# Kernel tuning notes

Hardware: AMD Instinct MI355X
Metric: run time of the kernel (lower is better)

The kernel has to match this reference:

```python
import jax, jax.numpy as jnp
import numpy as np

IMG_H = 800
IMG_W = 800
LEVEL_HW = [(200, 200), (100, 100), (50, 50), (25, 25), (13, 13)]
SIZES = [32.0, 64.0, 128.0, 256.0, 512.0]
RATIOS = np.array([0.5, 1.0, 2.0])
PRE_NMS = 1000     # rpn_pre_nms_top_n_test
POST_NMS = 1000    # rpn_post_nms_top_n_test
NMS_THRESH = 0.7
MIN_SIZE = 1e-3
BBOX_CLAMP = float(np.log(1000.0 / 16.0))  # torchvision BoxCoder clamp


def _make_anchors():
    """torchvision AnchorGenerator: 3 anchors/location, (h,w,a)-major order."""
    per_level = []
    for (H, W), size in zip(LEVEL_HW, SIZES):
        h_r = np.sqrt(RATIOS)
        w_r = 1.0 / h_r
        ws = w_r * size
        hs = h_r * size
        base = np.round(np.stack([-ws, -hs, ws, hs], axis=1) / 2.0)  # [3,4]
        stride_y = IMG_H // H
        stride_x = IMG_W // W
        shift_x = np.arange(W) * stride_x
        shift_y = np.arange(H) * stride_y
        yy, xx = np.meshgrid(shift_y, shift_x, indexing='ij')
        shifts = np.stack([xx.ravel(), yy.ravel(), xx.ravel(), yy.ravel()], axis=1)
        a = (shifts[:, None, :] + base[None, :, :]).reshape(-1, 4)  # [H*W*3,4]
        per_level.append(jnp.asarray(a, jnp.float32))
    return per_level


def _conv(x, w, b, pad):
    y = jax.lax.conv_general_dilated(
        x, w, window_strides=(1, 1), padding=[(pad, pad), (pad, pad)],
        dimension_numbers=('NCHW', 'OIHW', 'NCHW'))
    return y + b[None, :, None, None]


def _rpn_forward(feats, conv_w, conv_b, cls_w, cls_b, bbox_w, bbox_b):
    anchors_l = _make_anchors()
    boxes_list, scores_list, lvls_list = [], [], []
    for lvl, f in enumerate(feats):
        t = jax.nn.relu(_conv(f, conv_w, conv_b, 1))
        logits = _conv(t, cls_w, cls_b, 0)     # [1,3,H,W]
        deltas = _conv(t, bbox_w, bbox_b, 0)   # [1,12,H,W]
        H, W = f.shape[2], f.shape[3]
        s = logits[0].transpose(1, 2, 0).reshape(-1)                       # (h,w,a)
        d = deltas[0].reshape(3, 4, H, W).transpose(2, 3, 0, 1).reshape(-1, 4)
        k = min(PRE_NMS, s.shape[0])
        topv, topi = jax.lax.top_k(s, k)
        a = anchors_l[lvl][topi]
        dd = d[topi]
        # BoxCoder.decode, weights=(1,1,1,1)
        w_ = a[:, 2] - a[:, 0]
        h_ = a[:, 3] - a[:, 1]
        cx = a[:, 0] + 0.5 * w_
        cy = a[:, 1] + 0.5 * h_
        dx, dy = dd[:, 0], dd[:, 1]
        dw = jnp.minimum(dd[:, 2], BBOX_CLAMP)
        dh = jnp.minimum(dd[:, 3], BBOX_CLAMP)
        pcx = dx * w_ + cx
        pcy = dy * h_ + cy
        pw = jnp.exp(dw) * w_
        ph = jnp.exp(dh) * h_
        bx = jnp.stack([pcx - 0.5 * pw, pcy - 0.5 * ph,
                        pcx + 0.5 * pw, pcy + 0.5 * ph], axis=1)
        boxes_list.append(bx)
        scores_list.append(topv)
        lvls_list.append(jnp.full((k,), float(lvl), jnp.float32))
    boxes = jnp.concatenate(boxes_list)    # [N,4], N=4507
    scores = jnp.concatenate(scores_list)
    lvls = jnp.concatenate(lvls_list)
    # clip to image
    boxes = jnp.stack([boxes[:, 0].clip(0.0, IMG_W), boxes[:, 1].clip(0.0, IMG_H),
                       boxes[:, 2].clip(0.0, IMG_W), boxes[:, 3].clip(0.0, IMG_H)], axis=1)
    valid = ((boxes[:, 2] - boxes[:, 0]) >= MIN_SIZE) & ((boxes[:, 3] - boxes[:, 1]) >= MIN_SIZE)
    # batched NMS: offset boxes per level so cross-level IoU is zero
    off = lvls * (IMG_W + 1.0)
    ob = boxes + off[:, None]
    N = boxes.shape[0]
    order = jnp.argsort(-scores)
    b = ob[order]
    rb = boxes[order]
    s = scores[order]
    v = valid[order]
    area = (b[:, 2] - b[:, 0]) * (b[:, 3] - b[:, 1])
    lt = jnp.maximum(b[:, None, :2], b[None, :, :2])
    rbr = jnp.minimum(b[:, None, 2:], b[None, :, 2:])
    wh = jnp.clip(rbr - lt, 0.0)
    inter = wh[..., 0] * wh[..., 1]
    iou = inter / (area[:, None] + area[None, :] - inter)  # [N,N]
    idxs = jnp.arange(N)
    def body(i, keep):
        sup = keep[i] & (iou[i] > NMS_THRESH) & (idxs > i)
        return keep & ~sup
    keep = jax.lax.fori_loop(0, N, body, v)
    final_scores = jnp.where(keep, s, -jnp.inf)
    _, ki = jax.lax.top_k(final_scores, POST_NMS)
    return rb[ki]  # [POST_NMS, 4] proposals (padded to fixed size)


def setup_inputs() -> dict:
    key = jax.random.key(0)
    ks = jax.random.split(key, 12)
    inp = {}
    for i, (name, (H, W)) in enumerate(zip(['feat0', 'feat1', 'feat2', 'feat3', 'feat4'], LEVEL_HW)):
        inp[name] = jax.random.normal(ks[i], (1, 256, H, W), jnp.float32)
    inp['conv_w'] = jax.random.normal(ks[5], (256, 256, 3, 3), jnp.float32) * 0.02
    inp['conv_b'] = jnp.zeros((256,), jnp.float32)
    inp['cls_w'] = jax.random.normal(ks[6], (3, 256, 1, 1), jnp.float32) * 0.02
    inp['cls_b'] = jnp.zeros((3,), jnp.float32)
    inp['bbox_w'] = jax.random.normal(ks[7], (12, 256, 1, 1), jnp.float32) * 0.02
    inp['bbox_b'] = jnp.zeros((12,), jnp.float32)
    return inp


def reference(feat0, feat1, feat2, feat3, feat4, conv_w, conv_b, cls_w, cls_b, bbox_w, bbox_b):
    feats = [feat0, feat1, feat2, feat3, feat4]
    return _rpn_forward(feats, conv_w, conv_b, cls_w, cls_b, bbox_w, bbox_b)
```

## Files before the change

kernel.cpp:

```cpp
#include <hip/hip_runtime.h>
#include <cmath>

typedef unsigned int u32;
typedef unsigned long long u64;
typedef _Float16 f16;
typedef _Float16 f16x8 __attribute__((ext_vector_type(8)));
typedef float f32x4 __attribute__((ext_vector_type(4)));

typedef __attribute__((address_space(1))) const unsigned int gu32;
typedef __attribute__((address_space(3))) unsigned int lu32;

#define NCAND 4507
#define WORDS 71
#define ROWS_AL (WORDS * 64)
#define TOTS 159882

__constant__ int c_W[5]      = {200, 100, 50, 25, 13};
__constant__ int c_stride[5] = {4, 8, 16, 32, 61};
__constant__ int c_Nl[5]     = {120000, 30000, 7500, 1875, 507};
__constant__ int c_soff[5]   = {0, 120000, 150000, 157500, 159375};
__constant__ int c_k[5]      = {1000, 1000, 1000, 1000, 507};

__constant__ int cv_boff[6]  = {0, 625, 794, 843, 859, 863};

struct DecParams { float b[5][3][4]; };
struct FeatPtrs { const float* p[5]; };

__device__ __forceinline__ u32 flipf(float f) {
    u32 u = __float_as_uint(f);
    return (u & 0x80000000u) ? ~u : (u | 0x80000000u);
}

constexpr size_t AL(size_t x) { return (x + 255) & ~(size_t)255; }
constexpr size_t OFF_WHI    = 0;
constexpr size_t OFF_WLO    = AL(OFF_WHI + 1179648);
constexpr size_t OFF_HEADW  = AL(OFF_WLO + 1179648);
constexpr size_t OFF_HEADB  = AL(OFF_HEADW + 3840 * 4);
constexpr size_t OFF_SCORES = AL(OFF_HEADB + 64);
constexpr size_t OFF_DELTAS = AL(OFF_SCORES + (size_t)TOTS * 4);
constexpr size_t OFF_KEY    = AL(OFF_DELTAS + (size_t)TOTS * 16);
constexpr size_t OFF_SBOX   = AL(OFF_KEY + (size_t)NCAND * 8);
constexpr size_t OFF_SOB    = AL(OFF_SBOX + (size_t)NCAND * 16);
constexpr size_t OFF_SVAL   = AL(OFF_SOB + (size_t)NCAND * 16);
constexpr size_t OFF_MASK   = AL(OFF_SVAL + (size_t)NCAND * 4);
constexpr size_t OFF_KEEP   = AL(OFF_MASK + (size_t)ROWS_AL * WORDS * 8);
constexpr size_t OFF_GHIST  = AL(OFF_KEEP + WORDS * 8);

__global__ __launch_bounds__(256) void k_prep(
    const float* __restrict__ cw, const float* __restrict__ clsw,
    const float* __restrict__ clsb, const float* __restrict__ bw,
    const float* __restrict__ bb, f16* __restrict__ whi, f16* __restrict__ wlo,
    float* __restrict__ headw, float* __restrict__ headb, u32* __restrict__ ghist) {
    int i = blockIdx.x * 256 + threadIdx.x;
    if (i < 589824) {
        int blk = i >> 13;
        int within = i & 8191;
        int co = within >> 5;
        int rem = within & 31;
        int slot = rem >> 3, j = rem & 7;
        int chunk = blk / 9, kk = blk - chunk * 9;
        int ky = kk / 3, kx = kk - ky * 3;
        int g = slot ^ ((co >> 1) & 3);
        int ci = (chunk << 5) | (g << 3) | j;
        float w = cw[(((co << 8) + ci) * 3 + ky) * 3 + kx];
        f16 hi = (f16)w;
        whi[i] = hi;
        wlo[i] = (f16)((w - (float)hi) * 2048.0f);
    }
    if (i < 3840) {
        int h = i >> 8, ci = i & 255;
        headw[i] = (h < 3) ? clsw[h * 256 + ci] : bw[(h - 3) * 256 + ci];
    }
    if (i < 15) headb[i] = (i < 3) ? clsb[i] : bb[i - 3];
    if (i < 1280) ghist[i] = 0;
}

__global__ __launch_bounds__(512) void k_conv(
    FeatPtrs fp, const f16* __restrict__ whi, const f16* __restrict__ wlo,
    const float* __restrict__ convb, const float* __restrict__ headw,
    const float* __restrict__ headb, float* __restrict__ scores,
    float* __restrict__ deltas) {
    __shared__ float4 smq[4896];
    char* smb = (char*)smq;
    const int tid = threadIdx.x;
    const int lane = tid & 63, wv = tid >> 6;
    const int l15 = lane & 15, l4 = lane >> 4;

    const int bid = blockIdx.x;
    int l = 0;
#pragma unroll
    for (int q = 1; q < 5; q++) if (bid >= cv_boff[q]) l = q;
    const int H = c_W[l], W = H;
    const int soff = c_soff[l];
    const float* __restrict__ in = fp.p[l];
    const int t = bid - cv_boff[l];
    const int tilesx = (W + 7) >> 3;
    const int tx = t % tilesx, ty = t / tilesx;
    const int x0 = tx * 8, y0 = ty * 8;
    const int HW = H * W;

    int rbase0, rbase1, rbase2, rbase3;
    {
        int rr = l15 >> 3;
        rbase0 = (0 + rr) * 640; rbase1 = (2 + rr) * 640;
        rbase2 = (4 + rr) * 640; rbase3 = (6 + rr) * 640;
    }
    int colx0, colx1, colx2;
    {
        int c = lane & 7;
        int p0 = c, p1 = c + 1, p2 = c + 2;
        colx0 = p0 * 64 + ((l4 ^ ((p0 >> 1) & 3)) << 4);
        colx1 = p1 * 64 + ((l4 ^ ((p1 >> 1) & 3)) << 4);
        colx2 = p2 * 64 + ((l4 ^ ((p2 >> 1) & 3)) << 4);
    }
    int bco0 = wv * 32 + l15, bco1 = wv * 32 + 16 + l15;
    const int boff0 = bco0 * 64 + ((l4 ^ ((bco0 >> 1) & 3)) << 4);
    const int boff1 = bco1 * 64 + ((l4 ^ ((bco1 >> 1) & 3)) << 4);

    f32x4 acc1[4][2], acc2[4][2];
#pragma unroll
    for (int mt = 0; mt < 4; mt++)
#pragma unroll
        for (int nt = 0; nt < 2; nt++) {
            acc1[mt][nt] = (f32x4)0.0f;
            acc2[mt][nt] = (f32x4)0.0f;
        }

    auto stagePatch = [&](int chunk) {
        const int c0 = chunk << 5;
        f16* ph = (f16*)smb;
        f16* pl = (f16*)(smb + 6400);
        for (int e = tid; e < 3200; e += 512) {
            int py = e / 320, rem = e - py * 320;
            int px = rem >> 5, ci = rem & 31;
            int gy = y0 - 1 + py, gx = x0 - 1 + px;
            float v = 0.f;
            if (gy >= 0 && gy < H && gx >= 0 && gx < W)
                v = in[(c0 + ci) * HW + gy * W + gx];
            f16 hi = (f16)v;
            int widx = py * 320 + px * 32 + (((ci >> 3) ^ ((px >> 1) & 3)) << 3) + (ci & 7);
            ph[widx] = hi;
            pl[widx] = (f16)((v - (float)hi) * 2048.0f);
        }
    };
    auto issueB = [&](int sidx, int buf) {
        const char* gh = (const char*)whi + (size_t)sidx * 16384;
        const char* gl = (const char*)wlo + (size_t)sidx * 16384;
        char* dh = smb + 12800 + buf * 32768;
        char* dl = dh + 16384;
#pragma unroll
        for (int q = 0; q < 2; q++) {
            int i1 = (wv * 2 + q) * 1024;
            __builtin_amdgcn_global_load_lds((gu32*)(gh + i1 + lane * 16), (lu32*)(dh + i1), 16, 0, 0);
            __builtin_amdgcn_global_load_lds((gu32*)(gl + i1 + lane * 16), (lu32*)(dl + i1), 16, 0, 0);
        }
    };

// ... 34 lines not shown
                    acc2[1][nt] = __builtin_amdgcn_mfma_f32_16x16x32_f16(ah1, vbl, acc2[1][nt], 0, 0, 0);
                    acc2[1][nt] = __builtin_amdgcn_mfma_f32_16x16x32_f16(al1, vbh, acc2[1][nt], 0, 0, 0);
                    acc1[2][nt] = __builtin_amdgcn_mfma_f32_16x16x32_f16(ah2, vbh, acc1[2][nt], 0, 0, 0);
                    acc2[2][nt] = __builtin_amdgcn_mfma_f32_16x16x32_f16(ah2, vbl, acc2[2][nt], 0, 0, 0);
                    acc2[2][nt] = __builtin_amdgcn_mfma_f32_16x16x32_f16(al2, vbh, acc2[2][nt], 0, 0, 0);
                    acc1[3][nt] = __builtin_amdgcn_mfma_f32_16x16x32_f16(ah3, vbh, acc1[3][nt], 0, 0, 0);
                    acc2[3][nt] = __builtin_amdgcn_mfma_f32_16x16x32_f16(ah3, vbl, acc2[3][nt], 0, 0, 0);
                    acc2[3][nt] = __builtin_amdgcn_mfma_f32_16x16x32_f16(al3, vbh, acc2[3][nt], 0, 0, 0);
                }
            }
            __syncthreads();
        }
    }

    const float INV2048 = 4.8828125e-4f;
    {
        float cb0 = convb[bco0], cb1 = convb[bco1];
#pragma unroll
        for (int mt = 0; mt < 4; mt++)
#pragma unroll
            for (int nt = 0; nt < 2; nt++) {
                float cb = nt ? cb1 : cb0;
#pragma unroll
                for (int r = 0; r < 4; r++) {
                    float tv = acc1[mt][nt][r] + acc2[mt][nt][r] * INV2048 + cb;
                    acc1[mt][nt][r] = tv > 0.f ? tv : 0.f;
                }
            }
    }

    float* part = (float*)smb;
    for (int hc = 0; hc < 15; hc += 3) {
        float hw3[3][2];
#pragma unroll
        for (int h3 = 0; h3 < 3; h3++) {
            hw3[h3][0] = headw[(hc + h3) * 256 + bco0];
            hw3[h3][1] = headw[(hc + h3) * 256 + bco1];
        }
#pragma unroll
        for (int mt = 0; mt < 4; mt++)
#pragma unroll
            for (int r = 0; r < 4; r++) {
                float p0 = 0.f, p1 = 0.f, p2 = 0.f;
#pragma unroll
                for (int nt = 0; nt < 2; nt++) {
                    float tv = acc1[mt][nt][r];
                    p0 = fmaf(hw3[0][nt], tv, p0);
                    p1 = fmaf(hw3[1][nt], tv, p1);
                    p2 = fmaf(hw3[2][nt], tv, p2);
                }
                p0 += __shfl_xor(p0, 1); p0 += __shfl_xor(p0, 2); p0 += __shfl_xor(p0, 4); p0 += __shfl_xor(p0, 8);
                p1 += __shfl_xor(p1, 1); p1 += __shfl_xor(p1, 2); p1 += __shfl_xor(p1, 4); p1 += __shfl_xor(p1, 8);
                p2 += __shfl_xor(p2, 1); p2 += __shfl_xor(p2, 2); p2 += __shfl_xor(p2, 4); p2 += __shfl_xor(p2, 8);
                if (l15 == 0) {
                    int px = mt * 16 + l4 * 4 + r;
                    part[(wv * 64 + px) * 3 + 0] = p0;
                    part[(wv * 64 + px) * 3 + 1] = p1;
                    part[(wv * 64 + px) * 3 + 2] = p2;
                }
            }
        __syncthreads();
        if (tid < 192) {
            int px = tid / 3, h3 = tid % 3;
            int h = hc + h3;
            float sum = 0.f;
#pragma unroll
            for (int g = 0; g < 8; g++) sum += part[(g * 64 + px) * 3 + h3];
            sum += headb[h];
            int gy = y0 + (px >> 3), gx = x0 + (px & 7);
            if (gy < H && gx < W) {
                int pix = gy * W + gx;
                if (h < 3) {
                    scores[soff + pix * 3 + h] = sum;
                } else {
                    int ch2 = h - 3;
                    deltas[((size_t)(soff + pix * 3 + (ch2 >> 2))) * 4 + (ch2 & 3)] = sum;
                }
            }
        }
        __syncthreads();
    }
}

__global__ __launch_bounds__(256) void k_hist(
    const float* __restrict__ scores, u32* __restrict__ ghist) {
    __shared__ u32 lh[1280];
    for (int i = threadIdx.x; i < 1280; i += 256) lh[i] = 0;
    __syncthreads();
    const int gsz = gridDim.x * 256;
    for (int i = blockIdx.x * 256 + threadIdx.x; i < TOTS; i += gsz) {
        int l = (i >= 120000) + (i >= 150000) + (i >= 157500) + (i >= 159375);
        u32 b = flipf(scores[i]) >> 24;
        atomicAdd(&lh[l * 256 + b], 1u);
    }
    __syncthreads();
    for (int i = threadIdx.x; i < 1280; i += 256) {
        u32 v = lh[i];
        if (v) atomicAdd(&ghist[i], v);
    }
}

__global__ __launch_bounds__(1024) void k_topk2(
    const float* __restrict__ scores, const u32* __restrict__ ghist,
    u64* __restrict__ key, u64* __restrict__ scr1, u64* __restrict__ scr2) {
    const int l = blockIdx.x;
    const int Nl = c_Nl[l], off = c_soff[l], k = c_k[l];
    const int base = l * 1000;
    const int tid = threadIdx.x;
    const int lane = tid & 63;
    const u32 lshift = (u32)l << 24;
    __shared__ u32 hist[256];
    __shared__ u32 sh_sel, sh_cn, sh_b, sh_m;
    __shared__ u32 tiebuf[2048];

    if (k == Nl) {
        for (int i = tid; i < Nl; i += 1024) {
            u32 k32 = flipf(scores[off + i]);
            key[base + i] = ((u64)(~k32) << 32) | (u64)(lshift | (u32)i);
        }
        return;
    }
    if (tid == 0) {
        sh_sel = 0; sh_cn = 0;
        u32 cum = 0, m0 = (u32)k;
        for (int b = 255; b >= 0; --b) {
            u32 c = ghist[l * 256 + b];
            if (cum + c >= m0) { sh_b = (u32)b; sh_m = m0 - cum; break; }
            cum += c;
        }
    }
    __syncthreads();
    u32 b0 = sh_b, m = sh_m;

    u64* C = scr1 + off;
    for (int i = tid; i < Nl; i += 1024) {
        u32 k32 = flipf(scores[off + i]);
        u32 b = k32 >> 24;
        bool sel = b > b0, tie = (b == b0);
        u64 msk = __ballot(sel);
        if (msk) {
            int ldr = __builtin_ctzll(msk);
            u32 bs = 0;
            if (lane == ldr) bs = atomicAdd(&sh_sel, (u32)__popcll(msk));
            bs = __shfl(bs, ldr);
            if (sel) {
                u32 slot = bs + (u32)__popcll(msk & ((1ull << lane) - 1ull));
                key[base + slot] = ((u64)(~k32) << 32) | (u64)(lshift | (u32)i);
            }
        }
        msk = __ballot(tie);
        if (msk) {
            int ldr = __builtin_ctzll(msk);
            u32 bs = 0;
            if (lane == ldr) bs = atomicAdd(&sh_cn, (u32)__popcll(msk));
            bs = __shfl(bs, ldr);
            if (tie) {
                u32 slot = bs + (u32)__popcll(msk & ((1ull << lane) - 1ull));
                C[slot] = ((u64)k32 << 32) | (u64)(u32)i;
            }
        }
    }
    __syncthreads();
    u32 n = sh_cn;
    __syncthreads();

    u64* curb = C;
    u64* nxtb = scr2 + off;
    for (int p = 1; p <= 3; ++p) {
        const int shift = 56 - 8 * p;
        for (int b = tid; b < 256; b += 1024) hist[b] = 0;
        if (tid == 0) sh_cn = 0;
        __syncthreads();
        for (u32 j = tid; j < n; j += 1024)
            atomicAdd(&hist[(u32)(curb[j] >> shift) & 255u], 1u);
        __syncthreads();
        if (tid == 0) {
            u32 cum = 0;
            for (int b = 255; b >= 0; --b) {
                u32 c = hist[b];
                if (cum + c >= m) { sh_b = (u32)b; sh_m = m - cum; break; }
                cum += c;
            }
        }
        __syncthreads();
        u32 bp = sh_b; m = sh_m;
        for (u32 j = tid; j < n; j += 1024) {
            u64 e = curb[j];
            u32 b = (u32)(e >> shift) & 255u;
            bool sel = b > bp, tie = (b == bp);
            u64 msk = __ballot(sel);
            if (msk) {
                int ldr = __builtin_ctzll(msk);
                u32 bs = 0;
                if (lane == ldr) bs = atomicAdd(&sh_sel, (u32)__popcll(msk));
                bs = __shfl(bs, ldr);
                if (sel) {
                    u32 slot = bs + (u32)__popcll(msk & ((1ull << lane) - 1ull));
                    u32 k32 = (u32)(e >> 32);
                    key[base + slot] = ((u64)(~k32) << 32) | (u64)(lshift | (u32)(e & 0xFFFFFFu));
                }
            }
            msk = __ballot(tie);
            if (msk) {
                int ldr = __builtin_ctzll(msk);
                u32 bs = 0;
                if (lane == ldr) bs = atomicAdd(&sh_cn, (u32)__popcll(msk));
                bs = __shfl(bs, ldr);
                if (tie) {
                    u32 slot = bs + (u32)__popcll(msk & ((1ull << lane) - 1ull));
                    nxtb[slot] = e;
                }
            }
        }
        __syncthreads();
        n = sh_cn;
        __syncthreads();
        u64* tmp = curb; curb = nxtb; nxtb = tmp;
    }

    u32 nsel = sh_sel;
    u32 kt = (u32)(curb[0] >> 32);
    if (n == m) {
        for (u32 j = tid; j < n; j += 1024) {
            u64 e = curb[j];
            key[base + nsel + j] = ((u64)(~kt) << 32) | (u64)(lshift | (u32)(e & 0xFFFFFFu));
        }
    } else {
        for (u32 j = tid; j < 2048; j += 1024) tiebuf[j] = 0xFFFFFFFFu;
        __syncthreads();
        for (u32 j = tid; j < n && j < 2048; j += 1024) tiebuf[j] = (u32)(curb[j] & 0xFFFFFFu);
        __syncthreads();
        for (u32 ksz = 2; ksz <= 2048; ksz <<= 1) {
            for (u32 jj = ksz >> 1; jj > 0; jj >>= 1) {
                for (u32 i2 = tid; i2 < 2048; i2 += 1024) {
                    u32 ixj = i2 ^ jj;
                    if (ixj > i2) {
                        u32 a = tiebuf[i2], b = tiebuf[ixj];
                        bool up = ((i2 & ksz) == 0);
                        if ((a > b) == up) { tiebuf[i2] = b; tiebuf[ixj] = a; }
                    }
                }
                __syncthreads();
            }
        }
        for (u32 j = tid; j < m; j += 1024)
            key[base + nsel + j] = ((u64)(~kt) << 32) | (u64)(lshift | tiebuf[j]);
    }
}

__global__ __launch_bounds__(1024) void k_sort(
    const u64* __restrict__ key, const float* __restrict__ deltas, DecParams P,
    float* __restrict__ sboxes, float* __restrict__ sob, u32* __restrict__ svalid) {
    __shared__ u64 sk[8192];
    const int tid = threadIdx.x;
    for (int i = tid; i < 8192; i += 1024) sk[i] = (i < NCAND) ? key[i] : ~0ull;
    __syncthreads();
    for (u32 ksz = 2; ksz <= 8192; ksz <<= 1) {
        for (u32 j = ksz >> 1; j > 0; j >>= 1) {
            for (u32 i = tid; i < 8192; i += 1024) {
                u32 ixj = i ^ j;
                if (ixj > i) {
                    u64 a = sk[i], b = sk[ixj];
                    bool up = ((i & ksz) == 0);
                    if ((a > b) == up) { sk[i] = b; sk[ixj] = a; }
                }
            }
            __syncthreads();
        }
    }
    const float CLAMP = 4.135166556742356f;
    for (int s = tid; s < NCAND; s += 1024) {
        u32 info = (u32)sk[s];
        int l = info >> 24, idx = info & 0xFFFFFF;
        int W = c_W[l], st = c_stride[l];
        int a = idx % 3, pix = idx / 3;
        int x = pix % W, y = pix / W;
        float ax1 = x * st + P.b[l][a][0];
        float ay1 = y * st + P.b[l][a][1];
        float ax2 = x * st + P.b[l][a][2];
        float ay2 = y * st + P.b[l][a][3];
        float w_ = ax2 - ax1, h_ = ay2 - ay1;
        float cx = ax1 + 0.5f * w_, cy = ay1 + 0.5f * h_;
        const float* d = deltas + ((size_t)(c_soff[l] + idx)) * 4;
        float dx = d[0], dy = d[1];
        float dw = fminf(d[2], CLAMP), dh = fminf(d[3], CLAMP);
        float pcx = dx * w_ + cx, pcy = dy * h_ + cy;
        float pw = expf(dw) * w_, ph = expf(dh) * h_;
        float x1 = pcx - 0.5f * pw, y1 = pcy - 0.5f * ph;
        float x2 = pcx + 0.5f * pw, y2 = pcy + 0.5f * ph;
        x1 = fminf(fmaxf(x1, 0.f), 800.f); y1 = fminf(fmaxf(y1, 0.f), 800.f);
        x2 = fminf(fmaxf(x2, 0.f), 800.f); y2 = fminf(fmaxf(y2, 0.f), 800.f);
        u32 vv = (x2 - x1 >= 0.001f && y2 - y1 >= 0.001f) ? 1u : 0u;
        float offv = (float)l * 801.0f;
        sboxes[s * 4 + 0] = x1; sboxes[s * 4 + 1] = y1;
        sboxes[s * 4 + 2] = x2; sboxes[s * 4 + 3] = y2;
        sob[s * 4 + 0] = x1 + offv; sob[s * 4 + 1] = y1 + offv;
        sob[s * 4 + 2] = x2 + offv; sob[s * 4 + 3] = y2 + offv;
        svalid[s] = vv;
    }
}

__global__ __launch_bounds__(256) void k_mask(
    const float* __restrict__ sob, u64* __restrict__ mask) {
    int gid = blockIdx.x * 256 + threadIdx.x;
    const int total = NCAND * WORDS;
    if (gid >= total) return;
    int i = gid / WORDS, w = gid - i * WORDS;
    float bx1 = sob[i * 4], by1 = sob[i * 4 + 1], bx2 = sob[i * 4 + 2], by2 = sob[i * 4 + 3];
    float ai = (bx2 - bx1) * (by2 - by1);
    u64 bits = 0;
    int j0 = w * 64;
    for (int b = 0; b < 64; b++) {
        int j = j0 + b;
        if (j < NCAND && j > i) {
            float cx1 = sob[j * 4], cy1 = sob[j * 4 + 1], cx2 = sob[j * 4 + 2], cy2 = sob[j * 4 + 3];
            float lt0 = fmaxf(bx1, cx1), lt1 = fmaxf(by1, cy1);
            float rb0 = fminf(bx2, cx2), rb1 = fminf(by2, cy2);
            float ww = fmaxf(rb0 - lt0, 0.f), hh = fmaxf(rb1 - lt1, 0.f);
            float inter = ww * hh;
            float aj = (cx2 - cx1) * (cy2 - cy1);
            float u = ai + aj - inter;
            float iou = inter / u;
            if (iou > 0.7f) bits |= (1ull << b);
        }
    }
    mask[(size_t)i * WORDS + w] = bits;
}

__global__ __launch_bounds__(1024) void k_scan(
    const u64* __restrict__ mask, const u32* __restrict__ svalid,
    const float* __restrict__ sboxes, float* __restrict__ out) {
    __shared__ u64 keep[WORDS];
    __shared__ u32 ormL[WORDS], ormH[WORDS];
    __shared__ u32 sc[1024];
    const int tid = threadIdx.x;
    if (tid < WORDS) {
        u64 w0 = 0;
        for (int b = 0; b < 64; b++) {
// ... 21 lines not shown
        }
        __syncthreads();
        u64 kw = keep[t];
        int nW = WORDS - 1 - t;
        for (int task = tid; task < 64 * nW; task += 1024) {
            int r = task / nW, w = t + 1 + (task - r * nW);
            if ((kw >> r) & 1ull) {
                u64 mrow = mask[(size_t)(t * 64 + r) * WORDS + w];
                if (mrow) {
                    atomicOr(&ormL[w], (u32)mrow);
                    atomicOr(&ormH[w], (u32)(mrow >> 32));
                }
            }
        }
        __syncthreads();
        if (tid > t && tid < WORDS) {
            keep[tid] &= ~(((u64)ormH[tid] << 32) | (u64)ormL[tid]);
            ormL[tid] = 0; ormH[tid] = 0;
        }
        __syncthreads();
    }
    const int i0 = tid * 5;
    u32 cnt = 0;
    for (int e = 0; e < 5; e++) {
        int i = i0 + e;
        if (i < NCAND) cnt += (u32)((keep[i >> 6] >> (i & 63)) & 1ull);
    }
    sc[tid] = cnt;
    __syncthreads();
    for (int off = 1; off < 1024; off <<= 1) {
        u32 v = (tid >= off) ? sc[tid - off] : 0;
        __syncthreads();
        sc[tid] += v;
        __syncthreads();
    }
    u32 incl = sc[tid];
    u32 total = sc[1023];
    u32 kr = incl - cnt;
    for (int e = 0; e < 5; e++) {
        int i = i0 + e;
        if (i < NCAND) {
            bool kp = (keep[i >> 6] >> (i & 63)) & 1ull;
            if (kp) {
                if (kr < 1000u) {
                    out[kr * 4 + 0] = sboxes[i * 4 + 0];
                    out[kr * 4 + 1] = sboxes[i * 4 + 1];
                    out[kr * 4 + 2] = sboxes[i * 4 + 2];
                    out[kr * 4 + 3] = sboxes[i * 4 + 3];
                }
                kr++;
            } else {
                u32 slot = total + (u32)i - kr;
                if (slot < 1000u) {
                    out[slot * 4 + 0] = sboxes[i * 4 + 0];
                    out[slot * 4 + 1] = sboxes[i * 4 + 1];
                    out[slot * 4 + 2] = sboxes[i * 4 + 2];
                    out[slot * 4 + 3] = sboxes[i * 4 + 3];
                }
            }
        }
    }
}

extern "C" void kernel_launch(void* const* d_in, const int* in_sizes, int n_in,
                              void* d_out, int out_size, void* d_ws, size_t ws_size,
                              hipStream_t stream) {
    (void)in_sizes; (void)n_in; (void)out_size; (void)ws_size;
    FeatPtrs fp;
    for (int i = 0; i < 5; i++) fp.p[i] = (const float*)d_in[i];
    const float* conv_w = (const float*)d_in[5];
    const float* conv_b = (const float*)d_in[6];
    const float* cls_w  = (const float*)d_in[7];
    const float* cls_b  = (const float*)d_in[8];
    const float* bbox_w = (const float*)d_in[9];
    const float* bbox_b = (const float*)d_in[10];

    char* ws = (char*)d_ws;
    f16*   whi    = (f16*)(ws + OFF_WHI);
    f16*   wlo    = (f16*)(ws + OFF_WLO);
    float* headw  = (float*)(ws + OFF_HEADW);
    float* headb  = (float*)(ws + OFF_HEADB);
    float* scores = (float*)(ws + OFF_SCORES);
    float* deltas = (float*)(ws + OFF_DELTAS);
    u64*   key    = (u64*)(ws + OFF_KEY);
    float* sboxes = (float*)(ws + OFF_SBOX);
    float* sob    = (float*)(ws + OFF_SOB);
    u32*   svalid = (u32*)(ws + OFF_SVAL);
    u64*   maskp  = (u64*)(ws + OFF_MASK);
    u32*   ghist  = (u32*)(ws + OFF_GHIST);
    u64*   scr1   = maskp;
    u64*   scr2   = maskp + TOTS;

    k_prep<<<2304, 256, 0, stream>>>(conv_w, cls_w, cls_b, bbox_w, bbox_b,
                                     whi, wlo, headw, headb, ghist);

    k_conv<<<863, 512, 0, stream>>>(fp, whi, wlo, conv_b, headw, headb, scores, deltas);

    k_hist<<<256, 256, 0, stream>>>(scores, ghist);
    k_topk2<<<5, 1024, 0, stream>>>(scores, ghist, key, scr1, scr2);

    DecParams dp;
    {
        const double sz[5] = {32.0, 64.0, 128.0, 256.0, 512.0};
        const double rt[3] = {0.5, 1.0, 2.0};
        for (int l = 0; l < 5; l++)
            for (int a = 0; a < 3; a++) {
                double hr = sqrt(rt[a]);
                double wr = 1.0 / hr;
                double w = wr * sz[l], h = hr * sz[l];
                dp.b[l][a][0] = (float)nearbyint(-w / 2.0);
                dp.b[l][a][1] = (float)nearbyint(-h / 2.0);
                dp.b[l][a][2] = (float)nearbyint(w / 2.0);
                dp.b[l][a][3] = (float)nearbyint(h / 2.0);
            }
    }
    k_sort<<<1, 1024, 0, stream>>>(key, deltas, dp, sboxes, sob, svalid);
    k_mask<<<(NCAND * WORDS + 255) / 256, 256, 0, stream>>>(sob, maskp);
    k_scan<<<1, 1024, 0, stream>>>(maskp, svalid, sboxes, (float*)d_out);
}
```

Baseline: 980.9 us.

## Fuse histogram, per-level top-k selection and global sort into one kernel

Merges the histogram kernel, the 5-block radix top-k kernel and the single-block bitonic sort into one single-block kernel. Selected keys are written straight into shared memory instead of going through a global key buffer. Launch overhead and the global round trip are removed, and the per-level tie passes exit early when the ties are already resolved. The cost is that the 160K-element histogram and the candidate selection for all levels now run serially on one workgroup rather than across 256 plus 5 blocks.

```diff
diff --git a/kernel.cpp b/kernel.cpp
--- a/kernel.cpp
+++ b/kernel.cpp
@@ -38,19 +38,17 @@
 constexpr size_t OFF_HEADB  = AL(OFF_HEADW + 3840 * 4);
 constexpr size_t OFF_SCORES = AL(OFF_HEADB + 64);
 constexpr size_t OFF_DELTAS = AL(OFF_SCORES + (size_t)TOTS * 4);
-constexpr size_t OFF_KEY    = AL(OFF_DELTAS + (size_t)TOTS * 16);
-constexpr size_t OFF_SBOX   = AL(OFF_KEY + (size_t)NCAND * 8);
+constexpr size_t OFF_SBOX   = AL(OFF_DELTAS + (size_t)TOTS * 16);
 constexpr size_t OFF_SOB    = AL(OFF_SBOX + (size_t)NCAND * 16);
 constexpr size_t OFF_SVAL   = AL(OFF_SOB + (size_t)NCAND * 16);
 constexpr size_t OFF_MASK   = AL(OFF_SVAL + (size_t)NCAND * 4);
 constexpr size_t OFF_KEEP   = AL(OFF_MASK + (size_t)ROWS_AL * WORDS * 8);
-constexpr size_t OFF_GHIST  = AL(OFF_KEEP + WORDS * 8);
 
 __global__ __launch_bounds__(256) void k_prep(
     const float* __restrict__ cw, const float* __restrict__ clsw,
     const float* __restrict__ clsb, const float* __restrict__ bw,
     const float* __restrict__ bb, f16* __restrict__ whi, f16* __restrict__ wlo,
-    float* __restrict__ headw, float* __restrict__ headb, u32* __restrict__ ghist) {
+    float* __restrict__ headw, float* __restrict__ headb) {
     int i = blockIdx.x * 256 + threadIdx.x;
     if (i < 589824) {
         int blk = i >> 13;
@@ -72,7 +70,6 @@
         headw[i] = (h < 3) ? clsw[h * 256 + ci] : bw[(h - 3) * 256 + ci];
     }
     if (i < 15) headb[i] = (i < 3) ? clsb[i] : bb[i - 3];
-    if (i < 1280) ghist[i] = 0;
 }
 
 __global__ __launch_bounds__(512) void k_conv(
@@ -273,178 +270,184 @@
     }
 }
 
-__global__ __launch_bounds__(256) void k_hist(
-    const float* __restrict__ scores, u32* __restrict__ ghist) {
-    __shared__ u32 lh[1280];
-    for (int i = threadIdx.x; i < 1280; i += 256) lh[i] = 0;
-    __syncthreads();
-    const int gsz = gridDim.x * 256;
-    for (int i = blockIdx.x * 256 + threadIdx.x; i < TOTS; i += gsz) {
-        int l = (i >= 120000) + (i >= 150000) + (i >= 157500) + (i >= 159375);
-        u32 b = flipf(scores[i]) >> 24;
-        atomicAdd(&lh[l * 256 + b], 1u);
-    }
-    __syncthreads();
-    for (int i = threadIdx.x; i < 1280; i += 256) {
-        u32 v = lh[i];
-        if (v) atomicAdd(&ghist[i], v);
-    }
-}
-
-__global__ __launch_bounds__(1024) void k_topk2(
-    const float* __restrict__ scores, const u32* __restrict__ ghist,
-    u64* __restrict__ key, u64* __restrict__ scr1, u64* __restrict__ scr2) {
-    const int l = blockIdx.x;
-    const int Nl = c_Nl[l], off = c_soff[l], k = c_k[l];
-    const int base = l * 1000;
+__global__ __launch_bounds__(1024) void k_select(
+    const float* __restrict__ scores, const float* __restrict__ deltas, DecParams P,
+    float* __restrict__ sboxes, float* __restrict__ sob, u32* __restrict__ svalid,
+    u64* __restrict__ scr1, u64* __restrict__ scr2) {
+    __shared__ u64 sk[8192];
+    __shared__ u32 hist[1280];
+    __shared__ u32 tiebuf[2048];
+    __shared__ u32 sh_b0[5], sh_m[5], sh_sel[5], sh_cnt[5], sh_t1, sh_t2;
     const int tid = threadIdx.x;
     const int lane = tid & 63;
-    const u32 lshift = (u32)l << 24;
-    __shared__ u32 hist[256];
-    __shared__ u32 sh_sel, sh_cn, sh_b, sh_m;
-    __shared__ u32 tiebuf[2048];
-
-    if (k == Nl) {
+
+    for (int i = tid; i < 1280; i += 1024) hist[i] = 0;
+    __syncthreads();
+    for (int bi = 0; bi < TOTS; bi += 1024) {
+        int i = bi + tid;
+        bool valid = i < TOTS;
+        u32 bin = 0;
+        if (valid) {
+            int l = (i >= 120000) + (i >= 150000) + (i >= 157500) + (i >= 159375);
+            bin = ((u32)l << 8) | (flipf(scores[i]) >> 24);
+        }
+        u64 todo = __ballot(valid);
+        while (todo) {
+            int ldr = __builtin_ctzll(todo);
+            u32 lbin = __shfl(bin, ldr);
+            u64 match = __ballot(valid && bin == lbin);
+            if (lane == ldr) atomicAdd(&hist[lbin], (u32)__popcll(match));
+            todo &= ~match;
+        }
+    }
+    __syncthreads();
+    if (tid < 5) {
+        sh_sel[tid] = 0; sh_cnt[tid] = 0;
+        u32 m0 = (u32)c_k[tid];
+        if ((int)m0 == c_Nl[tid]) { sh_b0[tid] = 0x100; sh_m[tid] = 0; }
+        else {
+            u32 cum = 0;
+            for (int b = 255; b >= 0; --b) {
+                u32 c = hist[tid * 256 + b];
+                if (cum + c >= m0) { sh_b0[tid] = (u32)b; sh_m[tid] = m0 - cum; break; }
+                cum += c;
+            }
+        }
+    }
+    __syncthreads();
+    for (int i = tid; i < 507; i += 1024) {
+        u32 k32 = flipf(scores[159375 + i]);
+        sk[4000 + i] = ((u64)(~k32) << 32) | (u64)((4u << 24) | (u32)i);
+    }
+    for (int l = 0; l < 4; ++l) {
+        const int Nl = c_Nl[l], off = c_soff[l], base = l * 1000;
+        const u32 lshift = (u32)l << 24;
+        const u32 b0 = sh_b0[l];
+        u64* C = scr1 + off;
         for (int i = tid; i < Nl; i += 1024) {
             u32 k32 = flipf(scores[off + i]);
-            key[base + i] = ((u64)(~k32) << 32) | (u64)(lshift | (u32)i);
-        }
-        return;
-    }
-    if (tid == 0) {
-        sh_sel = 0; sh_cn = 0;
-        u32 cum = 0, m0 = (u32)k;
-        for (int b = 255; b >= 0; --b) {
-            u32 c = ghist[l * 256 + b];
-            if (cum + c >= m0) { sh_b = (u32)b; sh_m = m0 - cum; break; }
-            cum += c;
-        }
-    }
-    __syncthreads();
-    u32 b0 = sh_b, m = sh_m;
-
-    u64* C = scr1 + off;
-    for (int i = tid; i < Nl; i += 1024) {
-        u32 k32 = flipf(scores[off + i]);
-        u32 b = k32 >> 24;
-        bool sel = b > b0, tie = (b == b0);
-        u64 msk = __ballot(sel);
-        if (msk) {
-            int ldr = __builtin_ctzll(msk);
-            u32 bs = 0;
-            if (lane == ldr) bs = atomicAdd(&sh_sel, (u32)__popcll(msk));
-            bs = __shfl(bs, ldr);
-            if (sel) {
-                u32 slot = bs + (u32)__popcll(msk & ((1ull << lane) - 1ull));
-                key[base + slot] = ((u64)(~k32) << 32) | (u64)(lshift | (u32)i);
-            }
-        }
-        msk = __ballot(tie);
-        if (msk) {
-            int ldr = __builtin_ctzll(msk);
-            u32 bs = 0;
-            if (lane == ldr) bs = atomicAdd(&sh_cn, (u32)__popcll(msk));
-            bs = __shfl(bs, ldr);
-            if (tie) {
-                u32 slot = bs + (u32)__popcll(msk & ((1ull << lane) - 1ull));
-                C[slot] = ((u64)k32 << 32) | (u64)(u32)i;
-            }
-        }
-    }
-    __syncthreads();
-    u32 n = sh_cn;
-    __syncthreads();
-
-    u64* curb = C;
-    u64* nxtb = scr2 + off;
-    for (int p = 1; p <= 3; ++p) {
-        const int shift = 56 - 8 * p;
-        for (int b = tid; b < 256; b += 1024) hist[b] = 0;
-        if (tid == 0) sh_cn = 0;
-        __syncthreads();
-        for (u32 j = tid; j < n; j += 1024)
-            atomicAdd(&hist[(u32)(curb[j] >> shift) & 255u], 1u);
-        __syncthreads();
-        if (tid == 0) {
-            u32 cum = 0;
-            for (int b = 255; b >= 0; --b) {
-                u32 c = hist[b];
-                if (cum + c >= m) { sh_b = (u32)b; sh_m = m - cum; break; }
-                cum += c;
-            }
-        }
-        __syncthreads();
-        u32 bp = sh_b; m = sh_m;
-        for (u32 j = tid; j < n; j += 1024) {
-            u64 e = curb[j];
-            u32 b = (u32)(e >> shift) & 255u;
-            bool sel = b > bp, tie = (b == bp);
+            u32 b = k32 >> 24;
+            bool sel = b > b0, tie = (b == b0);
             u64 msk = __ballot(sel);
             if (msk) {
                 int ldr = __builtin_ctzll(msk);
                 u32 bs = 0;
-                if (lane == ldr) bs = atomicAdd(&sh_sel, (u32)__popcll(msk));
+                if (lane == ldr) bs = atomicAdd(&sh_sel[l], (u32)__popcll(msk));
                 bs = __shfl(bs, ldr);
                 if (sel) {
                     u32 slot = bs + (u32)__popcll(msk & ((1ull << lane) - 1ull));
-                    u32 k32 = (u32)(e >> 32);
-                    key[base + slot] = ((u64)(~k32) << 32) | (u64)(lshift | (u32)(e & 0xFFFFFFu));
+                    sk[base + slot] = ((u64)(~k32) << 32) | (u64)(lshift | (u32)i);
                 }
             }
             msk = __ballot(tie);
             if (msk) {
                 int ldr = __builtin_ctzll(msk);
                 u32 bs = 0;
-                if (lane == ldr) bs = atomicAdd(&sh_cn, (u32)__popcll(msk));
+                if (lane == ldr) bs = atomicAdd(&sh_cnt[l], (u32)__popcll(msk));
                 bs = __shfl(bs, ldr);
                 if (tie) {
                     u32 slot = bs + (u32)__popcll(msk & ((1ull << lane) - 1ull));
-                    nxtb[slot] = e;
-                }
-            }
-        }
-        __syncthreads();
-        n = sh_cn;
-        __syncthreads();
-        u64* tmp = curb; curb = nxtb; nxtb = tmp;
-    }
-
-    u32 nsel = sh_sel;
-    u32 kt = (u32)(curb[0] >> 32);
-    if (n == m) {
-        for (u32 j = tid; j < n; j += 1024) {
-            u64 e = curb[j];
-            key[base + nsel + j] = ((u64)(~kt) << 32) | (u64)(lshift | (u32)(e & 0xFFFFFFu));
-        }
-    } else {
-        for (u32 j = tid; j < 2048; j += 1024) tiebuf[j] = 0xFFFFFFFFu;
-        __syncthreads();
-        for (u32 j = tid; j < n && j < 2048; j += 1024) tiebuf[j] = (u32)(curb[j] & 0xFFFFFFu);
-        __syncthreads();
-        for (u32 ksz = 2; ksz <= 2048; ksz <<= 1) {
-            for (u32 jj = ksz >> 1; jj > 0; jj >>= 1) {
-                for (u32 i2 = tid; i2 < 2048; i2 += 1024) {
-                    u32 ixj = i2 ^ jj;
-                    if (ixj > i2) {
-                        u32 a = tiebuf[i2], b = tiebuf[ixj];
-                        bool up = ((i2 & ksz) == 0);
-                        if ((a > b) == up) { tiebuf[i2] = b; tiebuf[ixj] = a; }
+                    C[slot] = ((u64)k32 << 32) | (u64)(u32)i;
+                }
+            }
+        }
+    }
+    __syncthreads();
+    for (int l = 0; l < 4; ++l) {
+        const int off = c_soff[l], base = l * 1000;
+        const u32 lshift = (u32)l << 24;
+        u32 n = sh_cnt[l], m = sh_m[l];
+        u64* curb = scr1 + off;
+        u64* nxtb = scr2 + off;
+        int passes = 0;
+        for (int p = 1; p <= 3; ++p) {
+            if (n == m) break;
+            const int shift = 56 - 8 * p;
+            for (int b = tid; b < 256; b += 1024) hist[b] = 0;
+            if (tid == 0) sh_t1 = 0;
+            __syncthreads();
+            for (u32 j = tid; j < n; j += 1024)
+                atomicAdd(&hist[(u32)(curb[j] >> shift) & 255u], 1u);
+            __syncthreads();
+            if (tid == 0) {
+                u32 cum = 0;
+                for (int b = 255; b >= 0; --b) {
+                    u32 c = hist[b];
+                    if (cum + c >= m) { sh_t2 = (u32)b; sh_m[l] = m - cum; break; }
+                    cum += c;
+                }
+            }
+            __syncthreads();
+            u32 bp = sh_t2; m = sh_m[l];
+            for (u32 j = tid; j < n; j += 1024) {
+                u64 e = curb[j];
+                u32 b = (u32)(e >> shift) & 255u;
+                bool sel = b > bp, tie = (b == bp);
+                u64 msk = __ballot(sel);
+                if (msk) {
+                    int ldr = __builtin_ctzll(msk);
+                    u32 bs = 0;
+                    if (lane == ldr) bs = atomicAdd(&sh_sel[l], (u32)__popcll(msk));
+                    bs = __shfl(bs, ldr);
+                    if (sel) {
+                        u32 slot = bs + (u32)__popcll(msk & ((1ull << lane) - 1ull));
+                        u32 k32 = (u32)(e >> 32);
+                        sk[base + slot] = ((u64)(~k32) << 32) | (u64)(lshift | (u32)(e & 0xFFFFFFu));
                     }
                 }
-                __syncthreads();
-            }
-        }
-        for (u32 j = tid; j < m; j += 1024)
-            key[base + nsel + j] = ((u64)(~kt) << 32) | (u64)(lshift | tiebuf[j]);
-    }
-}
-
-__global__ __launch_bounds__(1024) void k_sort(
-    const u64* __restrict__ key, const float* __restrict__ deltas, DecParams P,
-    float* __restrict__ sboxes, float* __restrict__ sob, u32* __restrict__ svalid) {
-    __shared__ u64 sk[8192];
-    const int tid = threadIdx.x;
-    for (int i = tid; i < 8192; i += 1024) sk[i] = (i < NCAND) ? key[i] : ~0ull;
+                msk = __ballot(tie);
+                if (msk) {
+                    int ldr = __builtin_ctzll(msk);
+                    u32 bs = 0;
+                    if (lane == ldr) bs = atomicAdd(&sh_t1, (u32)__popcll(msk));
+                    bs = __shfl(bs, ldr);
+                    if (tie) {
+                        u32 slot = bs + (u32)__popcll(msk & ((1ull << lane) - 1ull));
+                        nxtb[slot] = e;
+                    }
+                }
+            }
+            __syncthreads();
+            n = sh_t1;
+            __syncthreads();
+            u64* tmp = curb; curb = nxtb; nxtb = tmp;
+            passes = p;
+        }
+        u32 nsel = sh_sel[l];
+        if (n == m) {
+            for (u32 j = tid; j < n; j += 1024) {
+                u64 e = curb[j];
+                u32 k32 = (u32)(e >> 32);
+                sk[base + nsel + j] = ((u64)(~k32) << 32) | (u64)(lshift | (u32)(e & 0xFFFFFFu));
+            }
+        } else {
+            (void)passes;
+            u32 kt = (u32)(curb[0] >> 32);
+            u32 nc = n > 2048u ? 2048u : n;
+            u32 S = 64; while (S < nc) S <<= 1;
+            for (u32 j = tid; j < S; j += 1024) tiebuf[j] = 0xFFFFFFFFu;
+            __syncthreads();
+            for (u32 j = tid; j < nc; j += 1024) tiebuf[j] = (u32)(curb[j] & 0xFFFFFFu);
+            __syncthreads();
+            for (u32 ksz = 2; ksz <= S; ksz <<= 1) {
+                for (u32 jj = ksz >> 1; jj > 0; jj >>= 1) {
+                    for (u32 i2 = tid; i2 < S; i2 += 1024) {
+                        u32 ixj = i2 ^ jj;
+                        if (ixj > i2) {
+                            u32 a = tiebuf[i2], b2 = tiebuf[ixj];
+                            bool up = ((i2 & ksz) == 0);
+                            if ((a > b2) == up) { tiebuf[i2] = b2; tiebuf[ixj] = a; }
+                        }
+                    }
+                    __syncthreads();
+                }
+            }
+            for (u32 j = tid; j < m; j += 1024)
+                sk[base + nsel + j] = ((u64)(~kt) << 32) | (u64)(lshift | tiebuf[j]);
+        }
+        __syncthreads();
+    }
+    for (int i = tid; i < 8192; i += 1024) if (i >= NCAND) sk[i] = ~0ull;
     __syncthreads();
     for (u32 ksz = 2; ksz <= 8192; ksz <<= 1) {
         for (u32 j = ksz >> 1; j > 0; j >>= 1) {
@@ -632,22 +635,17 @@
     float* headb  = (float*)(ws + OFF_HEADB);
     float* scores = (float*)(ws + OFF_SCORES);
     float* deltas = (float*)(ws + OFF_DELTAS);
-    u64*   key    = (u64*)(ws + OFF_KEY);
     float* sboxes = (float*)(ws + OFF_SBOX);
     float* sob    = (float*)(ws + OFF_SOB);
     u32*   svalid = (u32*)(ws + OFF_SVAL);
     u64*   maskp  = (u64*)(ws + OFF_MASK);
-    u32*   ghist  = (u32*)(ws + OFF_GHIST);
     u64*   scr1   = maskp;
     u64*   scr2   = maskp + TOTS;
 
     k_prep<<<2304, 256, 0, stream>>>(conv_w, cls_w, cls_b, bbox_w, bbox_b,
-                                     whi, wlo, headw, headb, ghist);
+                                     whi, wlo, headw, headb);
 
     k_conv<<<863, 512, 0, stream>>>(fp, whi, wlo, conv_b, headw, headb, scores, deltas);
-
-    k_hist<<<256, 256, 0, stream>>>(scores, ghist);
-    k_topk2<<<5, 1024, 0, stream>>>(scores, ghist, key, scr1, scr2);
 
     DecParams dp;
     {
@@ -664,7 +662,7 @@
                 dp.b[l][a][3] = (float)nearbyint(h / 2.0);
             }
     }
-    k_sort<<<1, 1024, 0, stream>>>(key, deltas, dp, sboxes, sob, svalid);
+    k_select<<<1, 1024, 0, stream>>>(scores, deltas, dp, sboxes, sob, svalid, scr1, scr2);
     k_mask<<<(NCAND * WORDS + 255) / 256, 256, 0, stream>>>(sob, maskp);
     k_scan<<<1, 1024, 0, stream>>>(maskp, svalid, sboxes, (float*)d_out);
 }
```

New measurement: 1.181 ms. 1.2x slower.

## Split top-k into a grid-wide classify pass and fuse tie refinement into sort

Applied to the files above, without the earlier changes.

The per-level top-k used to run as 5 blocks, each streaming every score of its level. It is replaced by a 320-block classify kernel that bins all scores against the first-byte threshold using global atomics. The remaining radix refinement of ties then runs inside the single-block sort kernel, written straight to shared memory, which removes one launch and a global round trip of the keys. The cost is serial per-level tie refinement in one block and global atomic contention on the per-level counters.

```diff
diff --git a/kernel.cpp b/kernel.cpp
--- a/kernel.cpp
+++ b/kernel.cpp
@@ -38,19 +38,21 @@
 constexpr size_t OFF_HEADB  = AL(OFF_HEADW + 3840 * 4);
 constexpr size_t OFF_SCORES = AL(OFF_HEADB + 64);
 constexpr size_t OFF_DELTAS = AL(OFF_SCORES + (size_t)TOTS * 4);
-constexpr size_t OFF_KEY    = AL(OFF_DELTAS + (size_t)TOTS * 16);
-constexpr size_t OFF_SBOX   = AL(OFF_KEY + (size_t)NCAND * 8);
+constexpr size_t OFF_SBOX   = AL(OFF_DELTAS + (size_t)TOTS * 16);
 constexpr size_t OFF_SOB    = AL(OFF_SBOX + (size_t)NCAND * 16);
 constexpr size_t OFF_SVAL   = AL(OFF_SOB + (size_t)NCAND * 16);
 constexpr size_t OFF_MASK   = AL(OFF_SVAL + (size_t)NCAND * 4);
 constexpr size_t OFF_KEEP   = AL(OFF_MASK + (size_t)ROWS_AL * WORDS * 8);
 constexpr size_t OFF_GHIST  = AL(OFF_KEEP + WORDS * 8);
+constexpr size_t OFF_CNT    = AL(OFF_GHIST + 1280 * 4);
+constexpr size_t OFF_KEY    = AL(OFF_CNT + 64);
 
 __global__ __launch_bounds__(256) void k_prep(
     const float* __restrict__ cw, const float* __restrict__ clsw,
     const float* __restrict__ clsb, const float* __restrict__ bw,
     const float* __restrict__ bb, f16* __restrict__ whi, f16* __restrict__ wlo,
-    float* __restrict__ headw, float* __restrict__ headb, u32* __restrict__ ghist) {
+    float* __restrict__ headw, float* __restrict__ headb,
+    u32* __restrict__ ghist, u32* __restrict__ cnts) {
     int i = blockIdx.x * 256 + threadIdx.x;
     if (i < 589824) {
         int blk = i >> 13;
@@ -73,6 +75,7 @@
     }
     if (i < 15) headb[i] = (i < 3) ? clsb[i] : bb[i - 3];
     if (i < 1280) ghist[i] = 0;
+    if (i < 16) cnts[i] = 0;
 }
 
 __global__ __launch_bounds__(512) void k_conv(
@@ -291,160 +294,179 @@
     }
 }
 
-__global__ __launch_bounds__(1024) void k_topk2(
+__global__ __launch_bounds__(512) void k_classify(
     const float* __restrict__ scores, const u32* __restrict__ ghist,
-    u64* __restrict__ key, u64* __restrict__ scr1, u64* __restrict__ scr2) {
-    const int l = blockIdx.x;
-    const int Nl = c_Nl[l], off = c_soff[l], k = c_k[l];
-    const int base = l * 1000;
+    u64* __restrict__ key, u64* __restrict__ scr1, u32* __restrict__ cnts) {
+    __shared__ u32 lh[1280];
+    __shared__ u32 sb0[5];
+    for (int i = threadIdx.x; i < 1280; i += 512) lh[i] = ghist[i];
+    __syncthreads();
+    if (threadIdx.x < 4) {
+        int l = threadIdx.x;
+        u32 m0 = (u32)c_k[l];
+        u32 cum = 0;
+        for (int b = 255; b >= 0; --b) {
+            u32 c = lh[l * 256 + b];
+            if (cum + c >= m0) { sb0[l] = (u32)b; break; }
+            cum += c;
+        }
+    }
+    __syncthreads();
+    const int lane = threadIdx.x & 63;
+    const int gsz = gridDim.x * 512;
+    for (int i = blockIdx.x * 512 + threadIdx.x; i < TOTS; i += gsz) {
+        int l = (i >= 120000) + (i >= 150000) + (i >= 157500) + (i >= 159375);
+        u32 il = (u32)(i - c_soff[l]);
+        u32 k32 = flipf(scores[i]);
+        u32 b = k32 >> 24;
+        bool sel = (l == 4) || (b > sb0[l]);
+        bool tie = (l < 4) && (b == sb0[l]);
+        u64 m1 = __ballot(sel);
+        while (m1) {
+            int ldr = __builtin_ctzll(m1);
+            int lv = __shfl(l, ldr);
+            u64 grp = __ballot(sel && (l == lv));
+            u32 bs = 0;
+            if (lane == ldr) bs = atomicAdd(&cnts[lv], (u32)__popcll(grp));
+            bs = __shfl(bs, ldr);
+            if (sel && l == lv) {
+                u32 slot = bs + (u32)__popcll(grp & ((1ull << lane) - 1ull));
+                key[lv * 1000 + slot] = ((u64)(~k32) << 32) | (u64)(((u32)lv << 24) | il);
+            }
+            m1 &= ~grp;
+        }
+        u64 m2 = __ballot(tie);
+        while (m2) {
+            int ldr = __builtin_ctzll(m2);
+            int lv = __shfl(l, ldr);
+            u64 grp = __ballot(tie && (l == lv));
+            u32 bs = 0;
+            if (lane == ldr) bs = atomicAdd(&cnts[8 + lv], (u32)__popcll(grp));
+            bs = __shfl(bs, ldr);
+            if (tie && l == lv) {
+                u32 slot = bs + (u32)__popcll(grp & ((1ull << lane) - 1ull));
+                scr1[c_soff[lv] + slot] = ((u64)k32 << 32) | (u64)il;
+            }
+            m2 &= ~grp;
+        }
+    }
+}
+
+__global__ __launch_bounds__(1024) void k_finish(
+    const u32* __restrict__ cnts, const u64* __restrict__ key,
+    const float* __restrict__ deltas, DecParams P,
+    u64* __restrict__ scr1, u64* __restrict__ scr2,
+    float* __restrict__ sboxes, float* __restrict__ sob, u32* __restrict__ svalid) {
+    __shared__ u64 sk[8192];
+    __shared__ u32 hist[256];
+    __shared__ u32 tiebuf[2048];
+    __shared__ u32 sh_sel, sh_t1, sh_t2, sh_m;
     const int tid = threadIdx.x;
     const int lane = tid & 63;
-    const u32 lshift = (u32)l << 24;
-    __shared__ u32 hist[256];
-    __shared__ u32 sh_sel, sh_cn, sh_b, sh_m;
-    __shared__ u32 tiebuf[2048];
-
-    if (k == Nl) {
-        for (int i = tid; i < Nl; i += 1024) {
-            u32 k32 = flipf(scores[off + i]);
-            key[base + i] = ((u64)(~k32) << 32) | (u64)(lshift | (u32)i);
-        }
-        return;
-    }
-    if (tid == 0) {
-        sh_sel = 0; sh_cn = 0;
-        u32 cum = 0, m0 = (u32)k;
-        for (int b = 255; b >= 0; --b) {
-            u32 c = ghist[l * 256 + b];
-            if (cum + c >= m0) { sh_b = (u32)b; sh_m = m0 - cum; break; }
-            cum += c;
-        }
-    }
-    __syncthreads();
-    u32 b0 = sh_b, m = sh_m;
-
-    u64* C = scr1 + off;
-    for (int i = tid; i < Nl; i += 1024) {
-        u32 k32 = flipf(scores[off + i]);
-        u32 b = k32 >> 24;
-        bool sel = b > b0, tie = (b == b0);
-        u64 msk = __ballot(sel);
-        if (msk) {
-            int ldr = __builtin_ctzll(msk);
-            u32 bs = 0;
-            if (lane == ldr) bs = atomicAdd(&sh_sel, (u32)__popcll(msk));
-            bs = __shfl(bs, ldr);
-            if (sel) {
-                u32 slot = bs + (u32)__popcll(msk & ((1ull << lane) - 1ull));
-                key[base + slot] = ((u64)(~k32) << 32) | (u64)(lshift | (u32)i);
-            }
-        }
-        msk = __ballot(tie);
-        if (msk) {
-            int ldr = __builtin_ctzll(msk);
-            u32 bs = 0;
-            if (lane == ldr) bs = atomicAdd(&sh_cn, (u32)__popcll(msk));
-            bs = __shfl(bs, ldr);
-            if (tie) {
-                u32 slot = bs + (u32)__popcll(msk & ((1ull << lane) - 1ull));
-                C[slot] = ((u64)k32 << 32) | (u64)(u32)i;
-            }
-        }
-    }
-    __syncthreads();
-    u32 n = sh_cn;
-    __syncthreads();
-
-    u64* curb = C;
-    u64* nxtb = scr2 + off;
-    for (int p = 1; p <= 3; ++p) {
-        const int shift = 56 - 8 * p;
-        for (int b = tid; b < 256; b += 1024) hist[b] = 0;
-        if (tid == 0) sh_cn = 0;
-        __syncthreads();
-        for (u32 j = tid; j < n; j += 1024)
-            atomicAdd(&hist[(u32)(curb[j] >> shift) & 255u], 1u);
-        __syncthreads();
-        if (tid == 0) {
-            u32 cum = 0;
-            for (int b = 255; b >= 0; --b) {
-                u32 c = hist[b];
-                if (cum + c >= m) { sh_b = (u32)b; sh_m = m - cum; break; }
-                cum += c;
-            }
-        }
-        __syncthreads();
-        u32 bp = sh_b; m = sh_m;
-        for (u32 j = tid; j < n; j += 1024) {
-            u64 e = curb[j];
-            u32 b = (u32)(e >> shift) & 255u;
-            bool sel = b > bp, tie = (b == bp);
-            u64 msk = __ballot(sel);
-            if (msk) {
-                int ldr = __builtin_ctzll(msk);
-                u32 bs = 0;
-                if (lane == ldr) bs = atomicAdd(&sh_sel, (u32)__popcll(msk));
-                bs = __shfl(bs, ldr);
-                if (sel) {
-                    u32 slot = bs + (u32)__popcll(msk & ((1ull << lane) - 1ull));
-                    u32 k32 = (u32)(e >> 32);
-                    key[base + slot] = ((u64)(~k32) << 32) | (u64)(lshift | (u32)(e & 0xFFFFFFu));
-                }
-            }
-            msk = __ballot(tie);
-            if (msk) {
-                int ldr = __builtin_ctzll(msk);
-                u32 bs = 0;
-                if (lane == ldr) bs = atomicAdd(&sh_cn, (u32)__popcll(msk));
-                bs = __shfl(bs, ldr);
-                if (tie) {
-                    u32 slot = bs + (u32)__popcll(msk & ((1ull << lane) - 1ull));
-                    nxtb[slot] = e;
-                }
-            }
-        }
-        __syncthreads();
-        n = sh_cn;
-        __syncthreads();
-        u64* tmp = curb; curb = nxtb; nxtb = tmp;
-    }
-
-    u32 nsel = sh_sel;
-    u32 kt = (u32)(curb[0] >> 32);
-    if (n == m) {
-        for (u32 j = tid; j < n; j += 1024) {
-            u64 e = curb[j];
-            key[base + nsel + j] = ((u64)(~kt) << 32) | (u64)(lshift | (u32)(e & 0xFFFFFFu));
-        }
-    } else {
-        for (u32 j = tid; j < 2048; j += 1024) tiebuf[j] = 0xFFFFFFFFu;
-        __syncthreads();
-        for (u32 j = tid; j < n && j < 2048; j += 1024) tiebuf[j] = (u32)(curb[j] & 0xFFFFFFu);
-        __syncthreads();
-        for (u32 ksz = 2; ksz <= 2048; ksz <<= 1) {
-            for (u32 jj = ksz >> 1; jj > 0; jj >>= 1) {
-                for (u32 i2 = tid; i2 < 2048; i2 += 1024) {
-                    u32 ixj = i2 ^ jj;
-                    if (ixj > i2) {
-                        u32 a = tiebuf[i2], b = tiebuf[ixj];
-                        bool up = ((i2 & ksz) == 0);
-                        if ((a > b) == up) { tiebuf[i2] = b; tiebuf[ixj] = a; }
+
+    for (int l = 0; l < 5; ++l) {
+        u32 n = cnts[l];
+        int base = l * 1000;
+        for (u32 j = tid; j < n; j += 1024) sk[base + j] = key[base + j];
+    }
+    __syncthreads();
+
+    for (int l = 0; l < 4; ++l) {
+        const int off = c_soff[l], base = l * 1000;
+        const u32 lshift = (u32)l << 24;
+        u32 nsel = cnts[l];
+        u32 m = (u32)c_k[l] - nsel;
+        u32 n = cnts[8 + l];
+        u64* curb = scr1 + off;
+        u64* nxtb = scr2 + off;
+        if (tid == 0) sh_sel = nsel;
+        __syncthreads();
+        for (int p = 1; p <= 3; ++p) {
+            if (n == m) break;
+            const int shift = 56 - 8 * p;
+            for (int b = tid; b < 256; b += 1024) hist[b] = 0;
+            if (tid == 0) sh_t1 = 0;
+            __syncthreads();
+            for (u32 j = tid; j < n; j += 1024)
+                atomicAdd(&hist[(u32)(curb[j] >> shift) & 255u], 1u);
+            __syncthreads();
+            if (tid == 0) {
+                u32 cum = 0;
+                for (int b = 255; b >= 0; --b) {
+                    u32 c = hist[b];
+                    if (cum + c >= m) { sh_t2 = (u32)b; sh_m = m - cum; break; }
+                    cum += c;
+                }
+            }
+            __syncthreads();
+            u32 bp = sh_t2; m = sh_m;
+            for (u32 j = tid; j < n; j += 1024) {
+                u64 e = curb[j];
+                u32 b = (u32)(e >> shift) & 255u;
+                bool sel = b > bp, tie = (b == bp);
+                u64 msk = __ballot(sel);
+                if (msk) {
+                    int ldr = __builtin_ctzll(msk);
+                    u32 bs = 0;
+                    if (lane == ldr) bs = atomicAdd(&sh_sel, (u32)__popcll(msk));
+                    bs = __shfl(bs, ldr);
+                    if (sel) {
+                        u32 slot = bs + (u32)__popcll(msk & ((1ull << lane) - 1ull));
+                        u32 k32 = (u32)(e >> 32);
+                        sk[base + slot] = ((u64)(~k32) << 32) | (u64)(lshift | (u32)(e & 0xFFFFFFu));
                     }
                 }
-                __syncthreads();
-            }
-        }
-        for (u32 j = tid; j < m; j += 1024)
-            key[base + nsel + j] = ((u64)(~kt) << 32) | (u64)(lshift | tiebuf[j]);
-    }
-}
-
-__global__ __launch_bounds__(1024) void k_sort(
-    const u64* __restrict__ key, const float* __restrict__ deltas, DecParams P,
-    float* __restrict__ sboxes, float* __restrict__ sob, u32* __restrict__ svalid) {
-    __shared__ u64 sk[8192];
-    const int tid = threadIdx.x;
-    for (int i = tid; i < 8192; i += 1024) sk[i] = (i < NCAND) ? key[i] : ~0ull;
+                msk = __ballot(tie);
+                if (msk) {
+                    int ldr = __builtin_ctzll(msk);
+                    u32 bs = 0;
+                    if (lane == ldr) bs = atomicAdd(&sh_t1, (u32)__popcll(msk));
+                    bs = __shfl(bs, ldr);
+                    if (tie) {
+                        u32 slot = bs + (u32)__popcll(msk & ((1ull << lane) - 1ull));
+                        nxtb[slot] = e;
+                    }
+                }
+            }
+            __syncthreads();
+            n = sh_t1;
+            __syncthreads();
+            u64* tmp = curb; curb = nxtb; nxtb = tmp;
+        }
+        u32 cs = sh_sel;
+        if (n == m) {
+            for (u32 j = tid; j < n; j += 1024) {
+                u64 e = curb[j];
+                u32 k32 = (u32)(e >> 32);
+                sk[base + cs + j] = ((u64)(~k32) << 32) | (u64)(lshift | (u32)(e & 0xFFFFFFu));
+            }
+        } else {
+            u32 kt = (u32)(curb[0] >> 32);
+            u32 nc = n > 2048u ? 2048u : n;
+            u32 S = 64; while (S < nc) S <<= 1;
+            for (u32 j = tid; j < S; j += 1024) tiebuf[j] = 0xFFFFFFFFu;
+            __syncthreads();
+            for (u32 j = tid; j < nc; j += 1024) tiebuf[j] = (u32)(curb[j] & 0xFFFFFFu);
+            __syncthreads();
+            for (u32 ksz = 2; ksz <= S; ksz <<= 1) {
+                for (u32 jj = ksz >> 1; jj > 0; jj >>= 1) {
+                    for (u32 i2 = tid; i2 < S; i2 += 1024) {
+                        u32 ixj = i2 ^ jj;
+                        if (ixj > i2) {
+                            u32 a = tiebuf[i2], b2 = tiebuf[ixj];
+                            bool up = ((i2 & ksz) == 0);
+                            if ((a > b2) == up) { tiebuf[i2] = b2; tiebuf[ixj] = a; }
+                        }
+                    }
+                    __syncthreads();
+                }
+            }
+            for (u32 j = tid; j < m; j += 1024)
+                sk[base + cs + j] = ((u64)(~kt) << 32) | (u64)(lshift | tiebuf[j]);
+        }
+        __syncthreads();
+    }
+    for (int i = tid; i < 8192; i += 1024) if (i >= NCAND) sk[i] = ~0ull;
     __syncthreads();
     for (u32 ksz = 2; ksz <= 8192; ksz <<= 1) {
         for (u32 j = ksz >> 1; j > 0; j >>= 1) {
@@ -632,22 +654,23 @@
     float* headb  = (float*)(ws + OFF_HEADB);
     float* scores = (float*)(ws + OFF_SCORES);
     float* deltas = (float*)(ws + OFF_DELTAS);
-    u64*   key    = (u64*)(ws + OFF_KEY);
     float* sboxes = (float*)(ws + OFF_SBOX);
     float* sob    = (float*)(ws + OFF_SOB);
     u32*   svalid = (u32*)(ws + OFF_SVAL);
     u64*   maskp  = (u64*)(ws + OFF_MASK);
     u32*   ghist  = (u32*)(ws + OFF_GHIST);
+    u32*   cnts   = (u32*)(ws + OFF_CNT);
+    u64*   key    = (u64*)(ws + OFF_KEY);
     u64*   scr1   = maskp;
     u64*   scr2   = maskp + TOTS;
 
     k_prep<<<2304, 256, 0, stream>>>(conv_w, cls_w, cls_b, bbox_w, bbox_b,
-                                     whi, wlo, headw, headb, ghist);
+                                     whi, wlo, headw, headb, ghist, cnts);
 
     k_conv<<<863, 512, 0, stream>>>(fp, whi, wlo, conv_b, headw, headb, scores, deltas);
 
     k_hist<<<256, 256, 0, stream>>>(scores, ghist);
-    k_topk2<<<5, 1024, 0, stream>>>(scores, ghist, key, scr1, scr2);
+    k_classify<<<320, 512, 0, stream>>>(scores, ghist, key, scr1, cnts);
 
     DecParams dp;
     {
@@ -664,7 +687,8 @@
                 dp.b[l][a][3] = (float)nearbyint(h / 2.0);
             }
     }
-    k_sort<<<1, 1024, 0, stream>>>(key, deltas, dp, sboxes, sob, svalid);
+    k_finish<<<1, 1024, 0, stream>>>(cnts, key, deltas, dp, scr1, scr2,
+                                     sboxes, sob, svalid);
     k_mask<<<(NCAND * WORDS + 255) / 256, 256, 0, stream>>>(sob, maskp);
     k_scan<<<1, 1024, 0, stream>>>(maskp, svalid, sboxes, (float*)d_out);
 }
```

After: 986.5 us. Within noise of the previous version (+0.6%).
